# Kernel tuning notes

Hardware: AMD Instinct MI355X
Metric: run time of the kernel (lower is better)

The kernel has to match this reference:

```python
import jax, jax.numpy as jnp
import numpy as np

O, I, B, G, BITS = 11008, 4096, 2048, 128, 3
N = I // G  # n_groups = 32
# Lloyd-Max optimal 8-level quantizer for unit Gaussian (3-bit PolarQuant codebook)
LLOYD_MAX_3BIT = [-2.1519, -1.3439, -0.7560, -0.2451, 0.2451, 0.7560, 1.3439, 2.1519]


def fwht(v):
    """Unnormalized fast Walsh-Hadamard transform along last axis (power-of-2 length)."""
    g = v.shape[-1]
    y = v.reshape(-1, g)
    h = 1
    while h < g:
        y = y.reshape(-1, g // (2 * h), 2, h)
        a, b = y[:, :, 0, :], y[:, :, 1, :]
        y = jnp.stack([a + b, a - b], axis=2).reshape(-1, g)
        h *= 2
    return y.reshape(v.shape)


def rotate(v, s1, s2):
    """Orthonormal randomized rotation R(v) = D2 * H * D1 * v / sqrt(G)."""
    g = v.shape[-1]
    return s2 * fwht(v * s1) * (1.0 / jnp.sqrt(jnp.asarray(g, v.dtype)))


def unpack3(packed):
    """Unpack 3-bit indices: [..., G//8*3] uint8 -> [..., G] int32 (matches unpack_indices)."""
    p = packed.reshape(*packed.shape[:-1], -1, 3).astype(jnp.int32)
    b0, b1, b2 = p[..., 0], p[..., 1], p[..., 2]
    outs = [
        b0 & 7, (b0 >> 3) & 7, ((b0 >> 6) | (b1 << 2)) & 7, (b1 >> 1) & 7,
        (b1 >> 4) & 7, ((b1 >> 7) | (b2 << 1)) & 7, (b2 >> 2) & 7, (b2 >> 5) & 7,
    ]
    return jnp.stack(outs, axis=-1).reshape(*packed.shape[:-1], -1)


def setup_inputs() -> dict:
    key = jax.random.key(0)
    kx, kw, k1, k2 = jax.random.split(key, 4)
    centroids = jnp.asarray(LLOYD_MAX_3BIT, dtype=jnp.float32)
    signs1 = jnp.where(jax.random.bernoulli(k1, 0.5, (G,)), 1.0, -1.0).astype(jnp.float32)
    signs2 = jnp.where(jax.random.bernoulli(k2, 0.5, (G,)), 1.0, -1.0).astype(jnp.float32)
    x = jax.random.normal(kx, (B, I), dtype=jnp.float32)
    # Quantize a dense weight exactly as TurboQuantWrapper.__init__ does.
    W = jax.random.normal(kw, (O, I), dtype=jnp.float32) * 0.02
    grouped = W.reshape(O, N, G)
    r = rotate(grouped, signs1, signs2)                     # [O,N,G] rotated groups
    gnorm = jnp.sqrt((r * r).sum(-1))                        # [O,N] (= ||w|| per group)
    dirn = r * jnp.sqrt(jnp.float32(G)) / (gnorm[..., None] + 1e-12)
    bnd = (centroids[:-1] + centroids[1:]) * 0.5
    idx = jnp.searchsorted(bnd, dirn)                        # nearest-centroid [O,N,G]
    q = centroids[idx]
    # norm correction: least-squares rescale of group norm against codebook hits
    norms = gnorm * (dirn * q).sum(-1) / ((q * q).sum(-1) + 1e-12)   # [O,N]
    # 3-bit packing: 8 indices -> 3 bytes (pack_indices, bits=3)
    v = np.asarray(idx, dtype=np.int32).reshape(O * N, G // 8, 8)
    b0 = v[..., 0] | (v[..., 1] << 3) | ((v[..., 2] & 3) << 6)
    b1 = (v[..., 2] >> 2) | (v[..., 3] << 1) | (v[..., 4] << 4) | ((v[..., 5] & 1) << 7)
    b2 = (v[..., 5] >> 1) | (v[..., 6] << 2) | (v[..., 7] << 5)
    packed = np.stack([b0, b1, b2], axis=-1).astype(np.uint8).reshape(O * N, G // 8 * 3)
    return {
        "x": x,
        "packed_weight": jnp.asarray(packed),
        "norms": norms.astype(jnp.float32),
        "centroids": centroids,
        "signs1": signs1,
        "signs2": signs2,
    }


def reference(x, packed_weight, norms, centroids, signs1, signs2):
    o, n = norms.shape
    g = signs1.shape[0]
    idx = unpack3(packed_weight.reshape(o, n, -1))           # [O,N,G] int32
    # FWHT-on-input: rotate each input group (fused kernel's input transform)
    rx = rotate(x.reshape(x.shape[0], n, g), signs1, signs2)  # [B,N,G]
    # Dequantized weight in rotated space: norm * centroid / sqrt(G)
    wq = centroids[idx] * (norms / jnp.sqrt(jnp.float32(g)))[:, :, None]  # [O,N,G]
    # x . w = R(x) . R(w) since R is orthonormal
    return jnp.einsum("bng,ong->bo", rx, wq)                 # [B,O]
```

## Files before the change

kernel.cpp:

```cpp
#include <hip/hip_runtime.h>

typedef unsigned int u32;
typedef unsigned short u16;

typedef short bf16x8 __attribute__((ext_vector_type(8)));
typedef float f32x4 __attribute__((ext_vector_type(4)));

#define GM 2048
#define GN 11008
#define GK 4096
#define NGRP 32
#define GSZ 128

#define CAST_G(p) ((const __attribute__((address_space(1))) void*)(p))
#define CAST_L(p) ((__attribute__((address_space(3))) void*)(p))
#define BAR() __builtin_amdgcn_s_barrier()
#define SCHED0() __builtin_amdgcn_sched_barrier(0)

__device__ __forceinline__ u16 f2bf(float f) {
    u32 u = __builtin_bit_cast(u32, f);
    u32 r = (u + 0x7FFFu + ((u >> 16) & 1u)) >> 16;
    return (u16)r;
}

__device__ __forceinline__ float cent3(int i) {
    int m3 = (i >= 4) ? (i - 4) : (3 - i);
    float mag = (m3 >= 2) ? ((m3 == 3) ? 2.1519f : 1.3439f)
                          : ((m3 == 1) ? 0.756f  : 0.2451f);
    return (i >= 4) ? mag : -mag;
}

#define ROT_BLOCKS (GM * NGRP / 4)
#define DQ_BLOCKS  (GN * NGRP * 4 / 256)

__global__ __launch_bounds__(256) void prep_kernel(
    const float* __restrict__ x, const float* __restrict__ s1,
    const float* __restrict__ s2, u32* __restrict__ rx,
    const u32* __restrict__ p32, const float* __restrict__ norms,
    u16* __restrict__ wq) {
    if (blockIdx.x < ROT_BLOCKS) {
        int gid  = blockIdx.x * 256 + threadIdx.x;
        int grp  = gid >> 6;
        int lane = gid & 63;

        const float2* xp = (const float2*)(x + (size_t)grp * GSZ);
        float2 xv  = xp[lane];
        float2 s1v = ((const float2*)s1)[lane];
        float2 s2v = ((const float2*)s2)[lane];

        float e0 = xv.x * s1v.x;
        float e1 = xv.y * s1v.y;
        {
            float a = e0 + e1, b = e0 - e1;
            e0 = a; e1 = b;
        }
        #pragma unroll
        for (int hb = 1; hb <= 32; hb <<= 1) {
            float t0 = __shfl_xor(e0, hb, 64);
            float t1 = __shfl_xor(e1, hb, 64);
            bool up = (lane & hb) != 0;
            e0 = up ? (t0 - e0) : (e0 + t0);
            e1 = up ? (t1 - e1) : (e1 + t1);
        }
        const float inv = 0.08838834764831845f;
        u32 lo = f2bf(e0 * s2v.x * inv);
        u32 hi = f2bf(e1 * s2v.y * inv);
        rx[gid] = lo | (hi << 16);
    } else {
        int u = (blockIdx.x - ROT_BLOCKS) * 256 + threadIdx.x;
        int g_idx = u >> 2;

        float scale = norms[g_idx] * 0.08838834764831845f;

        u32 w0 = p32[(size_t)u * 3 + 0];
        u32 w1 = p32[(size_t)u * 3 + 1];
        u32 w2 = p32[(size_t)u * 3 + 2];

        u32 tri[4];
        if (((w0 | w1 | w2) & 0xFFFFFF00u) == 0u) {
            const u32* pi = p32 + (size_t)u * 12;
            u32 b[12];
            #pragma unroll
            for (int k = 0; k < 12; ++k) b[k] = pi[k];
            #pragma unroll
            for (int t = 0; t < 4; ++t)
                tri[t] = b[3*t] | (b[3*t+1] << 8) | (b[3*t+2] << 16);
        } else {
            tri[0] = w0 & 0xFFFFFFu;
            tri[1] = (w0 >> 24) | ((w1 & 0xFFFFu) << 8);
            tri[2] = (w1 >> 16) | ((w2 & 0xFFu) << 16);
            tri[3] = w2 >> 8;
        }

        u32 ow[16];
        #pragma unroll
        for (int t = 0; t < 4; ++t) {
            u32 v = tri[t];
            #pragma unroll
            for (int k = 0; k < 4; ++k) {
                int i0 = (int)((v >> (6*k))     & 7u);
                int i1 = (int)((v >> (6*k + 3)) & 7u);
                u32 lo = f2bf(cent3(i0) * scale);
                u32 hi = f2bf(cent3(i1) * scale);
                ow[t*4 + k] = lo | (hi << 16);
            }
        }
        u32* op = (u32*)(wq + (size_t)u * 32);
        #pragma unroll
        for (int k = 0; k < 16; ++k) op[k] = ow[k];
    }
}

__device__ __forceinline__ void stage_half(const u16* g, char* ldst, int rowOff, int tt) {
    __builtin_amdgcn_global_load_lds(CAST_G(g + (size_t)rowOff * GK + tt * 64),
                                     CAST_L(ldst), 16, 0, 0);
    __builtin_amdgcn_global_load_lds(CAST_G(g + (size_t)(rowOff + 64) * GK + tt * 64),
                                     CAST_L(ldst + 8192), 16, 0, 0);
}

template<int AB_I, int BB_I>
__device__ __forceinline__ void ktile4(int t, char* lds,
                                       const u16* gA, const u16* gB,
                                       int sB, int aBase, int bBase, int sw0, int sw1,
                                       f32x4 (&acc)[8][4]) {
    const int AB  = AB_I * 32768;
    const int ABn = ((AB_I + 2) % 3) * 32768;
    const int BB  = 98304 + BB_I * 32768;
    const int BBo = 98304 + (BB_I ^ 1) * 32768;

    bf16x8 aF[4][2], b0F[2][2], b1F[2][2];
    bool s1 = (t < 63), s2 = (t < 62);

    #pragma unroll
    for (int mj = 0; mj < 4; ++mj) {
        aF[mj][0] = *(const bf16x8*)(lds + AB + aBase + mj * 4096 + sw0);
        aF[mj][1] = *(const bf16x8*)(lds + AB + aBase + mj * 4096 + sw1);
    }
    #pragma unroll
    for (int nj = 0; nj < 2; ++nj) {
        b0F[nj][0] = *(const bf16x8*)(lds + BB + bBase + nj * 8192 + sw0);
        b0F[nj][1] = *(const bf16x8*)(lds + BB + bBase + nj * 8192 + sw1);
    }
    #pragma unroll
    for (int nj = 0; nj < 2; ++nj) {
        b1F[nj][0] = *(const bf16x8*)(lds + BB + 16384 + bBase + nj * 8192 + sw0);
        b1F[nj][1] = *(const bf16x8*)(lds + BB + 16384 + bBase + nj * 8192 + sw1);
    }
    SCHED0();
    __builtin_amdgcn_s_setprio(1);
    #pragma unroll
    for (int kk = 0; kk < 2; ++kk) {
        #pragma unroll
        for (int mj = 0; mj < 4; ++mj)
            #pragma unroll
            for (int nj = 0; nj < 2; ++nj)
                acc[mj][nj] = __builtin_amdgcn_mfma_f32_16x16x32_bf16(
                    aF[mj][kk], b0F[nj][kk], acc[mj][nj], 0, 0, 0);
        #pragma unroll
        for (int mj = 0; mj < 4; ++mj)
            #pragma unroll
            for (int nj = 0; nj < 2; ++nj)
                acc[mj][2 + nj] = __builtin_amdgcn_mfma_f32_16x16x32_bf16(
                    aF[mj][kk], b1F[nj][kk], acc[mj][2 + nj], 0, 0, 0);
    }
    __builtin_amdgcn_s_setprio(0);
    if (s1) stage_half(gB, lds + BBo + 16384 + sB, 128, t + 1);
    if (s2) stage_half(gA, lds + ABn + sB,         0,   t + 2);
    BAR();

    #pragma unroll
    for (int mj = 0; mj < 4; ++mj) {
        aF[mj][0] = *(const bf16x8*)(lds + AB + 16384 + aBase + mj * 4096 + sw0);
        aF[mj][1] = *(const bf16x8*)(lds + AB + 16384 + aBase + mj * 4096 + sw1);
    }
    SCHED0();
    __builtin_amdgcn_s_setprio(1);
    #pragma unroll
    for (int kk = 0; kk < 2; ++kk) {
        #pragma unroll
        for (int mj = 0; mj < 4; ++mj)
            #pragma unroll
            for (int nj = 0; nj < 2; ++nj)
                acc[4 + mj][nj] = __builtin_amdgcn_mfma_f32_16x16x32_bf16(
                    aF[mj][kk], b0F[nj][kk], acc[4 + mj][nj], 0, 0, 0);
        #pragma unroll
        for (int mj = 0; mj < 4; ++mj)
            #pragma unroll
            for (int nj = 0; nj < 2; ++nj)
                acc[4 + mj][2 + nj] = __builtin_amdgcn_mfma_f32_16x16x32_bf16(
                    aF[mj][kk], b1F[nj][kk], acc[4 + mj][2 + nj], 0, 0, 0);
    }
    __builtin_amdgcn_s_setprio(0);
    if (s2) {
        stage_half(gB, lds + BB + sB,          0,   t + 2);
        stage_half(gA, lds + ABn + 16384 + sB, 128, t + 2);
    }
    if (s2) { asm volatile("s_waitcnt vmcnt(6)" ::: "memory"); }
    else    { asm volatile("s_waitcnt vmcnt(0)" ::: "memory"); }
    BAR();
}

__device__ __forceinline__ void gemm_big(int tau, int tid, char* lds,
                                         const u16* A, const u16* Bw, float* C) {
    int lane = tid & 63;
    int wv   = tid >> 6;
    int wr   = wv >> 2;
    int wc   = wv & 3;

    int n0 = (tau & 31) * 256;
    int m0 = (tau >> 5) * 256;

    int srow = tid >> 3;
    int c16  = (tid & 7) ^ (srow & 7);
    const u16* gA = A  + (size_t)(m0 + srow) * GK + c16 * 8;
    const u16* gB = Bw + (size_t)(n0 + srow) * GK + c16 * 8;
    int sB = wv * 1024;

    int aBase = (wr * 16 + (lane & 15)) * 128;
    int bBase = (wc * 16 + (lane & 15)) * 128;
    int sw0 = (((lane >> 4))     ^ (lane & 7)) << 4;
    int sw1 = (((lane >> 4) + 4) ^ (lane & 7)) << 4;

    f32x4 acc[8][4] = {};

    stage_half(gA, lds + sB,                  0,   0);
    stage_half(gA, lds + 16384 + sB,          128, 0);
    stage_half(gB, lds + 98304 + sB,          0,   0);
    stage_half(gB, lds + 98304 + 16384 + sB,  128, 0);
    stage_half(gA, lds + 32768 + sB,          0,   1);
    stage_half(gA, lds + 32768 + 16384 + sB,  128, 1);
    stage_half(gB, lds + 131072 + sB,         0,   1);
    asm volatile("s_waitcnt vmcnt(6)" ::: "memory");
    BAR();

    for (int tt = 0; tt < 60; tt += 6) {
        ktile4<0,0>(tt,     lds, gA, gB, sB, aBase, bBase, sw0, sw1, acc);
        ktile4<1,1>(tt + 1, lds, gA, gB, sB, aBase, bBase, sw0, sw1, acc);
        ktile4<2,0>(tt + 2, lds, gA, gB, sB, aBase, bBase, sw0, sw1, acc);
        ktile4<0,1>(tt + 3, lds, gA, gB, sB, aBase, bBase, sw0, sw1, acc);
        ktile4<1,0>(tt + 4, lds, gA, gB, sB, aBase, bBase, sw0, sw1, acc);
        ktile4<2,1>(tt + 5, lds, gA, gB, sB, aBase, bBase, sw0, sw1, acc);
    }
    ktile4<0,0>(60, lds, gA, gB, sB, aBase, bBase, sw0, sw1, acc);
    ktile4<1,1>(61, lds, gA, gB, sB, aBase, bBase, sw0, sw1, acc);
    ktile4<2,0>(62, lds, gA, gB, sB, aBase, bBase, sw0, sw1, acc);
    ktile4<0,1>(63, lds, gA, gB, sB, aBase, bBase, sw0, sw1, acc);

    int cr = (lane >> 4) * 4;
    int cc = lane & 15;
    #pragma unroll
    for (int mh = 0; mh < 2; ++mh)
        #pragma unroll
        for (int mj = 0; mj < 4; ++mj)
            #pragma unroll
            for (int nh = 0; nh < 2; ++nh)
                #pragma unroll
                for (int nj = 0; nj < 2; ++nj) {
                    float* cp = C + (size_t)(m0 + mh * 128 + wr * 16 + mj * 32 + cr) * GN
                                  + (n0 + nh * 128 + wc * 16 + nj * 64 + cc);
                    #pragma unroll
                    for (int j = 0; j < 4; ++j)
                        __builtin_nontemporal_store(acc[mh * 4 + mj][nh * 2 + nj][j],
                                                    cp + (size_t)j * GN);
                }
}

template<int BUF>
__device__ __forceinline__ void ktile2(int t, char* lds,
                                       const u16* gA, const u16* gB,
                                       int sB, int aBase, int bBase, int sw0, int sw1,
                                       f32x4 (&acc)[4][4]) {
    const int AB  = BUF * 16384;
    const int BB  = 49152 + BUF * 32768;
    const int NB  = (BUF + 2 >= 3) ? (BUF - 1) : (BUF + 2);
    const int ABn = NB * 16384;
    const int BBn = 49152 + NB * 32768;

    bf16x8 aF[4][2], bF[2][2];
    bool s2 = (t < 62);

    #pragma unroll
    for (int mj = 0; mj < 4; ++mj) {
        aF[mj][0] = *(const bf16x8*)(lds + AB + aBase + mj * 4096 + sw0);
        aF[mj][1] = *(const bf16x8*)(lds + AB + aBase + mj * 4096 + sw1);
    }
    #pragma unroll
    for (int nj = 0; nj < 2; ++nj) {
        bF[nj][0] = *(const bf16x8*)(lds + BB + bBase + nj * 8192 + sw0);
        bF[nj][1] = *(const bf16x8*)(lds + BB + bBase + nj * 8192 + sw1);
    }
    SCHED0();
    __builtin_amdgcn_s_setprio(1);
    #pragma unroll
    for (int kk = 0; kk < 2; ++kk)
        #pragma unroll
        for (int mj = 0; mj < 4; ++mj)
            #pragma unroll
            for (int nj = 0; nj < 2; ++nj)
                acc[mj][nj] = __builtin_amdgcn_mfma_f32_16x16x32_bf16(
                    aF[mj][kk], bF[nj][kk], acc[mj][nj], 0, 0, 0);
    __builtin_amdgcn_s_setprio(0);
    if (s2) {
        stage_half(gA, lds + ABn + sB, 0, t + 2);
        stage_half(gB, lds + BBn + sB, 0, t + 2);
    }
    BAR();

    #pragma unroll
    for (int nj = 0; nj < 2; ++nj) {
        bF[nj][0] = *(const bf16x8*)(lds + BB + 16384 + bBase + nj * 8192 + sw0);
        bF[nj][1] = *(const bf16x8*)(lds + BB + 16384 + bBase + nj * 8192 + sw1);
    }
    SCHED0();
    __builtin_amdgcn_s_setprio(1);
    #pragma unroll
    for (int kk = 0; kk < 2; ++kk)
        #pragma unroll
        for (int mj = 0; mj < 4; ++mj)
            #pragma unroll
            for (int nj = 0; nj < 2; ++nj)
                acc[mj][2 + nj] = __builtin_amdgcn_mfma_f32_16x16x32_bf16(
                    aF[mj][kk], bF[nj][kk], acc[mj][2 + nj], 0, 0, 0);
    __builtin_amdgcn_s_setprio(0);
    if (s2) stage_half(gB, lds + BBn + 16384 + sB, 128, t + 2);
    if (s2) { asm volatile("s_waitcnt vmcnt(6)" ::: "memory"); }
    else    { asm volatile("s_waitcnt vmcnt(0)" ::: "memory"); }
    BAR();
}

__device__ __forceinline__ void gemm_tail(int bid, int tid, char* lds,
                                          const u16* A, const u16* Bw, float* C) {
    int lane = tid & 63;
    int wv   = tid >> 6;
    int wr   = wv >> 2;
    int wc   = wv & 3;

    int x = bid & 7, s = bid >> 3;
    int nt, mh;
    if (s < 16) { nt = x; mh = s; }
    else { int idx = (s - 16) * 8 + x; nt = 8 + (idx >> 4); mh = idx & 15; }
    int m0  = mh * 128;
    int n0  = 8192 + nt * 256;

    int srow = tid >> 3;
    int c16  = (tid & 7) ^ (srow & 7);
    const u16* gA = A  + (size_t)(m0 + srow) * GK + c16 * 8;
    const u16* gB = Bw + (size_t)(n0 + srow) * GK + c16 * 8;
    int sB = wv * 1024;

    int aBase = (wr * 16 + (lane & 15)) * 128;
    int bBase = (wc * 16 + (lane & 15)) * 128;
    int sw0 = (((lane >> 4))     ^ (lane & 7)) << 4;
    int sw1 = (((lane >> 4) + 4) ^ (lane & 7)) << 4;

    f32x4 acc[4][4] = {};

    stage_half(gA, lds + sB,                 0,   0);
    stage_half(gB, lds + 49152 + sB,         0,   0);
    stage_half(gB, lds + 49152 + 16384 + sB, 128, 0);
    stage_half(gA, lds + 16384 + sB,         0,   1);
    stage_half(gB, lds + 81920 + sB,         0,   1);
    stage_half(gB, lds + 81920 + 16384 + sB, 128, 1);
    asm volatile("s_waitcnt vmcnt(6)" ::: "memory");
    BAR();

    for (int tt = 0; tt < 63; tt += 3) {
        ktile2<0>(tt,     lds, gA, gB, sB, aBase, bBase, sw0, sw1, acc);
        ktile2<1>(tt + 1, lds, gA, gB, sB, aBase, bBase, sw0, sw1, acc);
        ktile2<2>(tt + 2, lds, gA, gB, sB, aBase, bBase, sw0, sw1, acc);
    }
    ktile2<0>(63, lds, gA, gB, sB, aBase, bBase, sw0, sw1, acc);

    int cr = (lane >> 4) * 4;
    int cc = lane & 15;
    #pragma unroll
    for (int mj = 0; mj < 4; ++mj)
        #pragma unroll
        for (int nj = 0; nj < 4; ++nj) {
            float* cp = C + (size_t)(m0 + wr * 16 + mj * 32 + cr) * GN
                          + (n0 + wc * 16 + nj * 64 + cc);
            #pragma unroll
            for (int j = 0; j < 4; ++j)
                __builtin_nontemporal_store(acc[mj][nj][j], cp + (size_t)j * GN);
        }
}

__global__ __launch_bounds__(512, 1) void gemm_all_kernel(
    const u16* __restrict__ A, const u16* __restrict__ Bw,
    float* __restrict__ C) {
    extern __shared__ char lds[];
    int bid = blockIdx.x;
    if (bid < 256) gemm_big (bid,       threadIdx.x, lds, A, Bw, C);
    else           gemm_tail(bid - 256, threadIdx.x, lds, A, Bw, C);
}

extern "C" void kernel_launch(void* const* d_in, const int* in_sizes, int n_in,
                              void* d_out, int out_size, void* d_ws, size_t ws_size,
                              hipStream_t stream) {
    const float* x      = (const float*)d_in[0];
    const void*  packed = d_in[1];
    const float* norms  = (const float*)d_in[2];
    const float* s1     = (const float*)d_in[4];
    const float* s2     = (const float*)d_in[5];
    float* out          = (float*)d_out;

    size_t rx_bytes = (size_t)GM * GK * 2;
    size_t wq_bytes = (size_t)GN * GK * 2;
    if (ws_size < rx_bytes + wq_bytes) return;

    u16* rx = (u16*)d_ws;
    u16* wq = rx + (size_t)GM * GK;

    prep_kernel<<<dim3(ROT_BLOCKS + DQ_BLOCKS), dim3(256), 0, stream>>>(
        x, s1, s2, (u32*)rx, (const u32*)packed, norms, wq);

    hipFuncSetAttribute((const void*)gemm_all_kernel,
                        hipFuncAttributeMaxDynamicSharedMemorySize, 163840);
    gemm_all_kernel<<<dim3(432), dim3(512), 163840, stream>>>(rx, wq, out);
}
```

Baseline: 203.3 us.

## Switch big GEMM tile to 32x32x16 MFMA with reworked fragment layout

Replaces the 16x16x32 bf16 MFMA inner loop of the 256x256 GEMM tile with 32x32x16 MFMAs. Per-wave accumulators become 4x2 sixteen-wide vectors, and the LDS fragment addressing, XOR swizzle and output store mapping are redone to match. The larger instruction is meant to cut LDS reads per FLOP and MFMA issue overhead. It risks LDS bank conflicts under the new swizzle and a less coalesced epilogue store pattern.

```diff
diff --git a/kernel.cpp b/kernel.cpp
--- a/kernel.cpp
+++ b/kernel.cpp
@@ -5,6 +5,7 @@
 
 typedef short bf16x8 __attribute__((ext_vector_type(8)));
 typedef float f32x4 __attribute__((ext_vector_type(4)));
+typedef float f32x16 __attribute__((ext_vector_type(16)));
 
 #define GM 2048
 #define GN 11008
@@ -119,77 +120,60 @@
 }
 
 template<int AB_I, int BB_I>
-__device__ __forceinline__ void ktile4(int t, char* lds,
-                                       const u16* gA, const u16* gB,
-                                       int sB, int aBase, int bBase, int sw0, int sw1,
-                                       f32x4 (&acc)[8][4]) {
+__device__ __forceinline__ void ktile32(int t, char* lds,
+                                        const u16* gA, const u16* gB,
+                                        int sB, int aBase, int bBase,
+                                        int sw0, int sw1, int sw2, int sw3,
+                                        f32x16 (&acc)[4][2]) {
     const int AB  = AB_I * 32768;
     const int ABn = ((AB_I + 2) % 3) * 32768;
     const int BB  = 98304 + BB_I * 32768;
     const int BBo = 98304 + (BB_I ^ 1) * 32768;
 
-    bf16x8 aF[4][2], b0F[2][2], b1F[2][2];
+    const int sw[4] = {sw0, sw1, sw2, sw3};
+    bf16x8 aF[2][4], bF[2][4];
     bool s1 = (t < 63), s2 = (t < 62);
 
     #pragma unroll
-    for (int mj = 0; mj < 4; ++mj) {
-        aF[mj][0] = *(const bf16x8*)(lds + AB + aBase + mj * 4096 + sw0);
-        aF[mj][1] = *(const bf16x8*)(lds + AB + aBase + mj * 4096 + sw1);
-    }
-    #pragma unroll
-    for (int nj = 0; nj < 2; ++nj) {
-        b0F[nj][0] = *(const bf16x8*)(lds + BB + bBase + nj * 8192 + sw0);
-        b0F[nj][1] = *(const bf16x8*)(lds + BB + bBase + nj * 8192 + sw1);
-    }
-    #pragma unroll
-    for (int nj = 0; nj < 2; ++nj) {
-        b1F[nj][0] = *(const bf16x8*)(lds + BB + 16384 + bBase + nj * 8192 + sw0);
-        b1F[nj][1] = *(const bf16x8*)(lds + BB + 16384 + bBase + nj * 8192 + sw1);
-    }
+    for (int mi = 0; mi < 2; ++mi)
+        #pragma unroll
+        for (int ks = 0; ks < 4; ++ks)
+            aF[mi][ks] = *(const bf16x8*)(lds + AB + aBase + mi * 4096 + sw[ks]);
+    #pragma unroll
+    for (int nh = 0; nh < 2; ++nh)
+        #pragma unroll
+        for (int ks = 0; ks < 4; ++ks)
+            bF[nh][ks] = *(const bf16x8*)(lds + BB + nh * 16384 + bBase + sw[ks]);
     SCHED0();
     __builtin_amdgcn_s_setprio(1);
     #pragma unroll
-    for (int kk = 0; kk < 2; ++kk) {
-        #pragma unroll
-        for (int mj = 0; mj < 4; ++mj)
-            #pragma unroll
-            for (int nj = 0; nj < 2; ++nj)
-                acc[mj][nj] = __builtin_amdgcn_mfma_f32_16x16x32_bf16(
-                    aF[mj][kk], b0F[nj][kk], acc[mj][nj], 0, 0, 0);
-        #pragma unroll
-        for (int mj = 0; mj < 4; ++mj)
-            #pragma unroll
-            for (int nj = 0; nj < 2; ++nj)
-                acc[mj][2 + nj] = __builtin_amdgcn_mfma_f32_16x16x32_bf16(
-                    aF[mj][kk], b1F[nj][kk], acc[mj][2 + nj], 0, 0, 0);
-    }
+    for (int ks = 0; ks < 4; ++ks)
+        #pragma unroll
+        for (int mi = 0; mi < 2; ++mi)
+            #pragma unroll
+            for (int nh = 0; nh < 2; ++nh)
+                acc[mi][nh] = __builtin_amdgcn_mfma_f32_32x32x16_bf16(
+                    aF[mi][ks], bF[nh][ks], acc[mi][nh], 0, 0, 0);
     __builtin_amdgcn_s_setprio(0);
     if (s1) stage_half(gB, lds + BBo + 16384 + sB, 128, t + 1);
     if (s2) stage_half(gA, lds + ABn + sB,         0,   t + 2);
     BAR();
 
     #pragma unroll
-    for (int mj = 0; mj < 4; ++mj) {
-        aF[mj][0] = *(const bf16x8*)(lds + AB + 16384 + aBase + mj * 4096 + sw0);
-        aF[mj][1] = *(const bf16x8*)(lds + AB + 16384 + aBase + mj * 4096 + sw1);
-    }
+    for (int mi = 0; mi < 2; ++mi)
+        #pragma unroll
+        for (int ks = 0; ks < 4; ++ks)
+            aF[mi][ks] = *(const bf16x8*)(lds + AB + 16384 + aBase + mi * 4096 + sw[ks]);
     SCHED0();
     __builtin_amdgcn_s_setprio(1);
     #pragma unroll
-    for (int kk = 0; kk < 2; ++kk) {
-        #pragma unroll
-        for (int mj = 0; mj < 4; ++mj)
-            #pragma unroll
-            for (int nj = 0; nj < 2; ++nj)
-                acc[4 + mj][nj] = __builtin_amdgcn_mfma_f32_16x16x32_bf16(
-                    aF[mj][kk], b0F[nj][kk], acc[4 + mj][nj], 0, 0, 0);
-        #pragma unroll
-        for (int mj = 0; mj < 4; ++mj)
-            #pragma unroll
-            for (int nj = 0; nj < 2; ++nj)
-                acc[4 + mj][2 + nj] = __builtin_amdgcn_mfma_f32_16x16x32_bf16(
-                    aF[mj][kk], b1F[nj][kk], acc[4 + mj][2 + nj], 0, 0, 0);
-    }
+    for (int ks = 0; ks < 4; ++ks)
+        #pragma unroll
+        for (int mi = 0; mi < 2; ++mi)
+            #pragma unroll
+            for (int nh = 0; nh < 2; ++nh)
+                acc[2 + mi][nh] = __builtin_amdgcn_mfma_f32_32x32x16_bf16(
+                    aF[mi][ks], bF[nh][ks], acc[2 + mi][nh], 0, 0, 0);
     __builtin_amdgcn_s_setprio(0);
     if (s2) {
         stage_half(gB, lds + BB + sB,          0,   t + 2);
@@ -216,12 +200,15 @@
     const u16* gB = Bw + (size_t)(n0 + srow) * GK + c16 * 8;
     int sB = wv * 1024;
 
-    int aBase = (wr * 16 + (lane & 15)) * 128;
-    int bBase = (wc * 16 + (lane & 15)) * 128;
-    int sw0 = (((lane >> 4))     ^ (lane & 7)) << 4;
-    int sw1 = (((lane >> 4) + 4) ^ (lane & 7)) << 4;
-
-    f32x4 acc[8][4] = {};
+    int aBase = (wr * 64 + (lane & 31)) * 128;
+    int bBase = (wc * 32 + (lane & 31)) * 128;
+    int l7 = lane & 7, l5 = lane >> 5;
+    int sw0 = ((0 + l5) ^ l7) << 4;
+    int sw1 = ((2 + l5) ^ l7) << 4;
+    int sw2 = ((4 + l5) ^ l7) << 4;
+    int sw3 = ((6 + l5) ^ l7) << 4;
+
+    f32x16 acc[4][2] = {};
 
     stage_half(gA, lds + sB,                  0,   0);
     stage_half(gA, lds + 16384 + sB,          128, 0);
@@ -234,35 +221,33 @@
     BAR();
 
     for (int tt = 0; tt < 60; tt += 6) {
-        ktile4<0,0>(tt,     lds, gA, gB, sB, aBase, bBase, sw0, sw1, acc);
-        ktile4<1,1>(tt + 1, lds, gA, gB, sB, aBase, bBase, sw0, sw1, acc);
-        ktile4<2,0>(tt + 2, lds, gA, gB, sB, aBase, bBase, sw0, sw1, acc);
-        ktile4<0,1>(tt + 3, lds, gA, gB, sB, aBase, bBase, sw0, sw1, acc);
-        ktile4<1,0>(tt + 4, lds, gA, gB, sB, aBase, bBase, sw0, sw1, acc);
-        ktile4<2,1>(tt + 5, lds, gA, gB, sB, aBase, bBase, sw0, sw1, acc);
-    }
-    ktile4<0,0>(60, lds, gA, gB, sB, aBase, bBase, sw0, sw1, acc);
-    ktile4<1,1>(61, lds, gA, gB, sB, aBase, bBase, sw0, sw1, acc);
-    ktile4<2,0>(62, lds, gA, gB, sB, aBase, bBase, sw0, sw1, acc);
-    ktile4<0,1>(63, lds, gA, gB, sB, aBase, bBase, sw0, sw1, acc);
-
-    int cr = (lane >> 4) * 4;
-    int cc = lane & 15;
-    #pragma unroll
-    for (int mh = 0; mh < 2; ++mh)
-        #pragma unroll
-        for (int mj = 0; mj < 4; ++mj)
-            #pragma unroll
-            for (int nh = 0; nh < 2; ++nh)
-                #pragma unroll
-                for (int nj = 0; nj < 2; ++nj) {
-                    float* cp = C + (size_t)(m0 + mh * 128 + wr * 16 + mj * 32 + cr) * GN
-                                  + (n0 + nh * 128 + wc * 16 + nj * 64 + cc);
-                    #pragma unroll
-                    for (int j = 0; j < 4; ++j)
-                        __builtin_nontemporal_store(acc[mh * 4 + mj][nh * 2 + nj][j],
-                                                    cp + (size_t)j * GN);
-                }
+        ktile32<0,0>(tt,     lds, gA, gB, sB, aBase, bBase, sw0, sw1, sw2, sw3, acc);
+        ktile32<1,1>(tt + 1, lds, gA, gB, sB, aBase, bBase, sw0, sw1, sw2, sw3, acc);
+        ktile32<2,0>(tt + 2, lds, gA, gB, sB, aBase, bBase, sw0, sw1, sw2, sw3, acc);
+        ktile32<0,1>(tt + 3, lds, gA, gB, sB, aBase, bBase, sw0, sw1, sw2, sw3, acc);
+        ktile32<1,0>(tt + 4, lds, gA, gB, sB, aBase, bBase, sw0, sw1, sw2, sw3, acc);
+        ktile32<2,1>(tt + 5, lds, gA, gB, sB, aBase, bBase, sw0, sw1, sw2, sw3, acc);
+    }
+    ktile32<0,0>(60, lds, gA, gB, sB, aBase, bBase, sw0, sw1, sw2, sw3, acc);
+    ktile32<1,1>(61, lds, gA, gB, sB, aBase, bBase, sw0, sw1, sw2, sw3, acc);
+    ktile32<2,0>(62, lds, gA, gB, sB, aBase, bBase, sw0, sw1, sw2, sw3, acc);
+    ktile32<0,1>(63, lds, gA, gB, sB, aBase, bBase, sw0, sw1, sw2, sw3, acc);
+
+    int cc = lane & 31;
+    int rofs = 4 * (lane >> 5);
+    #pragma unroll
+    for (int mg = 0; mg < 4; ++mg) {
+        int rb = m0 + (mg >> 1) * 128 + wr * 64 + (mg & 1) * 32 + rofs;
+        #pragma unroll
+        for (int nh = 0; nh < 2; ++nh) {
+            float* cp = C + (size_t)rb * GN + (n0 + nh * 128 + wc * 32 + cc);
+            #pragma unroll
+            for (int reg = 0; reg < 16; ++reg) {
+                int rr = (reg & 3) + 8 * (reg >> 2);
+                __builtin_nontemporal_store(acc[mg][nh][reg], cp + (size_t)rr * GN);
+            }
+        }
+    }
 }
 
 template<int BUF>
```

New measurement: 217.8 us. +7.1%, slower.
